# Kernel tuning notes

Measured on AMD Instinct MI355X. Metric: run time of the kernel, lower is better.

The kernel has to match this reference:

```python
import jax, jax.numpy as jnp
import numpy as np

NUM_NODES = 50000
NUM_EDGES = 800000
DIM = 64
NUM_REL2 = 400
NUM_LAYERS = 3
NUM_TAILS = 512


def setup_inputs() -> dict:
    key = jax.random.key(0)
    ks = jax.random.split(key, 16)
    s = lambda shape, k, scale: jax.random.normal(k, shape, jnp.float32) * scale
    return {
        'head_embeds': s((DIM,), ks[0], 1.0),
        'rel_table': s((NUM_REL2, DIM), ks[1], 0.1),
        'rel_W': s((NUM_LAYERS, NUM_REL2, DIM), ks[2], 0.1),
        'agg_W': s((NUM_LAYERS, 8 * DIM, DIM), ks[3], (8 * DIM) ** -0.5),
        'agg_b': jnp.zeros((NUM_LAYERS, DIM), jnp.float32),
        'lin_W': s((2 * DIM, DIM), ks[4], (2 * DIM) ** -0.5),
        'lin_b': jnp.zeros((DIM,), jnp.float32),
        'mlp_W1': s((DIM, 2 * DIM), ks[5], DIM ** -0.5),
        'mlp_b1': jnp.zeros((2 * DIM,), jnp.float32),
        'mlp_W2': s((2 * DIM, 1), ks[6], (2 * DIM) ** -0.5),
        'mlp_b2': jnp.zeros((1,), jnp.float32),
        'edge_src': jax.random.randint(ks[7], (NUM_EDGES,), 0, NUM_NODES, jnp.int32),
        'edge_dst': jax.random.randint(ks[8], (NUM_EDGES,), 0, NUM_NODES, jnp.int32),
        'edge_type': jax.random.randint(ks[9], (NUM_EDGES,), 0, NUM_REL2, jnp.int32),
        'head_index': 0,
        'r_index': 7,
        't_index': jax.random.randint(ks[10], (NUM_TAILS,), 0, NUM_NODES, jnp.int32),
    }


def _score_fn(hidden, query, lin_W, lin_b, mlp_W1, mlp_b1, mlp_W2, mlp_b2):
    # hidden: [N, d], query: [d]
    q = jnp.broadcast_to(query, hidden.shape)
    heuristic = jnp.concatenate([hidden, q], axis=-1) @ lin_W + lin_b  # [N, d]
    x = hidden * heuristic
    h1 = jax.nn.relu(x @ mlp_W1 + mlp_b1)
    return (h1 @ mlp_W2 + mlp_b2)[..., 0]  # [N]


def reference(head_embeds, rel_table, rel_W, agg_W, agg_b, lin_W, lin_b,
              mlp_W1, mlp_b1, mlp_W2, mlp_b2,
              edge_src, edge_dst, edge_type, head_index, r_index, t_index):
    N, d = NUM_NODES, DIM
    score_fn = lambda h, q: _score_fn(h, q, lin_W, lin_b, mlp_W1, mlp_b1, mlp_W2, mlp_b2)

    query = rel_table[r_index]  # [d]

    # init_input_embeds: boundary zeros except head node; init score
    hidden = jnp.zeros((N, d), jnp.float32).at[head_index].set(head_embeds)
    zero_s = score_fn(jnp.zeros((1, d), jnp.float32), query)[0]
    score = jnp.full((N,), zero_s, jnp.float32)
    score = score.at[head_index].set(score_fn(head_embeds[None, :], query)[0])
    score = jnp.clip(score, -15.0, 15.0)

    deg = jax.ops.segment_sum(jnp.ones_like(edge_dst, jnp.float32), edge_dst, N)  # [N]
    deg_safe = jnp.maximum(deg, 1.0)
    has_in = deg > 0
    pna_degree_mean = jnp.log(deg + 1.0).mean()
    scale = (jnp.log(deg + 1.0) / pna_degree_mean)[:, None]  # [N,1]

    for l in range(NUM_LAYERS):
        gate = jax.nn.sigmoid(score)[:, None]  # [N,1]
        layer_input = gate * hidden  # [N,d]
        # relational messages: gather + per-relation transform
        msg = layer_input[edge_src] * rel_W[l][edge_type]  # [E,d]
        # PNA aggregators per destination node
        ssum = jax.ops.segment_sum(msg, edge_dst, N)
        mean = ssum / deg_safe[:, None]
        sq = jax.ops.segment_sum(msg * msg, edge_dst, N) / deg_safe[:, None]
        std = jnp.sqrt(jnp.maximum(sq - mean * mean, 0.0) + 1e-6)
        mx = jax.ops.segment_max(msg, edge_dst, N)
        mn = jax.ops.segment_min(msg, edge_dst, N)
        mx = jnp.where(has_in[:, None], mx, 0.0)
        mn = jnp.where(has_in[:, None], mn, 0.0)
        feat = jnp.concatenate([mean, mx, mn, std], axis=-1)  # [N,4d]
        feat = jnp.concatenate([feat, feat * scale], axis=-1)  # [N,8d]
        update = feat @ agg_W[l] + agg_b[l]  # [N,d]
        # residual update only for nodes with incoming edges
        hidden = hidden + jnp.where(has_in[:, None], update, 0.0)
        new_score = score_fn(hidden, query)
        score = jnp.where(has_in, new_score, score)

    return score[t_index]  # [NUM_TAILS]
```

## Files before the change

kernel.cpp:

```cpp
#include <hip/hip_runtime.h>
#include <math.h>

#define NN 50000
#define NREL 400
#define NLAYERS 3

static __device__ __forceinline__ float clip15(float x) { return fminf(fmaxf(x, -15.f), 15.f); }

__global__ void count_k(const int* __restrict__ dst, int* __restrict__ deg, int E) {
  int e = blockIdx.x * blockDim.x + threadIdx.x;
  if (e < E) atomicAdd(&deg[dst[e]], 1);
}

__global__ void scan_k(const int* __restrict__ deg, int* __restrict__ start, int* __restrict__ cursor,
                       int* __restrict__ counter, float* __restrict__ logsum, int N) {
  int n = blockIdx.x * blockDim.x + threadIdx.x;
  int lane = threadIdx.x & 63;
  int d = (n < N) ? deg[n] : 0;
  int pre = d;
  #pragma unroll
  for (int off = 1; off < 64; off <<= 1) { int t = __shfl_up(pre, off); if (lane >= off) pre += t; }
  int base = 0;
  if (lane == 63) base = atomicAdd(counter, pre);
  base = __shfl(base, 63);
  if (n < N) { int pos = base + pre - d; start[n] = pos; cursor[n] = pos; }
  float v = (n < N) ? logf((float)d + 1.0f) : 0.f;
  #pragma unroll
  for (int off = 32; off; off >>= 1) v += __shfl_xor(v, off);
  if (lane == 0) atomicAdd(logsum, v);
}

__global__ void scale_k(const int* __restrict__ deg, const float* __restrict__ logsum,
                        float* __restrict__ scale, int N) {
  int n = blockIdx.x * blockDim.x + threadIdx.x;
  if (n < N) scale[n] = logf((float)deg[n] + 1.0f) * (float)N / logsum[0];
}

__global__ void scatter_k(const int* __restrict__ src, const int* __restrict__ dst,
                          const int* __restrict__ typ, int* __restrict__ cursor,
                          int2* __restrict__ csr, int E) {
  int e = blockIdx.x * blockDim.x + threadIdx.x;
  if (e < E) {
    int dd = dst[e];
    int pos = atomicAdd(&cursor[dd], 1);
    csr[pos] = make_int2(src[e], typ[e]);
  }
}

__global__ void prep_k(const float* __restrict__ head_embeds, const float* __restrict__ rel_table,
                       const float* __restrict__ lin_W, const float* __restrict__ lin_b,
                       const float* __restrict__ mlp_W1, const float* __restrict__ mlp_b1,
                       const float* __restrict__ mlp_W2, const float* __restrict__ mlp_b2,
                       const int* __restrict__ head_index, const int* __restrict__ r_index,
                       float* __restrict__ hidden, float* __restrict__ scalars) {
  int j = threadIdx.x;
  int r = r_index[0], hd = head_index[0];
  float qj = rel_table[r * 64 + j];
  float cq = lin_b[j];
  for (int k = 0; k < 64; ++k) cq += __shfl(qj, k) * lin_W[(64 + k) * 64 + j];
  scalars[j] = cq;
  float t = fmaxf(mlp_b1[j], 0.f) * mlp_W2[j] + fmaxf(mlp_b1[64 + j], 0.f) * mlp_W2[64 + j];
  #pragma unroll
  for (int off = 32; off; off >>= 1) t += __shfl_xor(t, off);
  float zs = clip15(t + mlp_b2[0]);
  float hj = head_embeds[j];
  hidden[(size_t)hd * 64 + j] = hj;
  float heur = cq;
  for (int k = 0; k < 64; ++k) heur += __shfl(hj, k) * lin_W[k * 64 + j];
  float xj = hj * heur;
  float h1a = mlp_b1[j], h1b = mlp_b1[64 + j];
  for (int k = 0; k < 64; ++k) {
    float xk = __shfl(xj, k);
    h1a += xk * mlp_W1[k * 128 + j];
    h1b += xk * mlp_W1[k * 128 + 64 + j];
  }
  h1a = fmaxf(h1a, 0.f); h1b = fmaxf(h1b, 0.f);
  float p = h1a * mlp_W2[j] + h1b * mlp_W2[64 + j];
  #pragma unroll
  for (int off = 32; off; off >>= 1) p += __shfl_xor(p, off);
  float hs = clip15(p + mlp_b2[0]);
  if (j == 0) { scalars[64] = zs; scalars[65] = hs; }
}

__global__ void fill_k(float* __restrict__ score, const float* __restrict__ scalars,
                       const int* __restrict__ head_index, int N) {
  int n = blockIdx.x * blockDim.x + threadIdx.x;
  if (n < N) score[n] = (n == head_index[0]) ? scalars[65] : scalars[64];
}

__global__ void gate_k(const float* __restrict__ hidden, const float* __restrict__ score,
                       float* __restrict__ LI, int N) {
  int i = blockIdx.x * blockDim.x + threadIdx.x;
  if (i < N * 16) {
    int node = i >> 4;
    float s = score[node];
    float g = 1.f / (1.f + expf(-s));
    float4 h = ((const float4*)hidden)[i];
    float4 r = make_float4(h.x * g, h.y * g, h.z * g, h.w * g);
    ((float4*)LI)[i] = r;
  }
}

__global__ __launch_bounds__(256) void agg_k(const float* __restrict__ LI, const int2* __restrict__ csr,
                                             const int* __restrict__ start, const int* __restrict__ deg,
                                             const float* __restrict__ relW, float* __restrict__ f1, int N) {
  int wid = threadIdx.x >> 6;
  int lane = threadIdx.x & 63;
  int node = blockIdx.x * 4 + wid;
  if (node >= N) return;
  int base = start[node], d = deg[node];
  float sum = 0.f, sq = 0.f, mx = -3.402823e38f, mn = 3.402823e38f;
  int e = 0;
  for (; e + 8 <= d; e += 8) {
    int2 p[8];
    #pragma unroll
    for (int i = 0; i < 8; ++i) p[i] = csr[base + e + i];
    float m[8];
    #pragma unroll
    for (int i = 0; i < 8; ++i) {
      float a = LI[p[i].x * 64 + lane];
      float w = relW[p[i].y * 64 + lane];
      m[i] = a * w;
    }
    #pragma unroll
    for (int i = 0; i < 8; ++i) {
      sum += m[i]; sq += m[i] * m[i];
      mx = fmaxf(mx, m[i]); mn = fminf(mn, m[i]);
    }
  }
  for (; e + 4 <= d; e += 4) {
    int2 p0 = csr[base + e], p1 = csr[base + e + 1];
    int2 p2 = csr[base + e + 2], p3 = csr[base + e + 3];
    float a0 = LI[p0.x * 64 + lane], w0 = relW[p0.y * 64 + lane];
    float a1 = LI[p1.x * 64 + lane], w1 = relW[p1.y * 64 + lane];
    float a2 = LI[p2.x * 64 + lane], w2 = relW[p2.y * 64 + lane];
    float a3 = LI[p3.x * 64 + lane], w3 = relW[p3.y * 64 + lane];
    float m0 = a0 * w0, m1 = a1 * w1, m2 = a2 * w2, m3 = a3 * w3;
    sum += (m0 + m1) + (m2 + m3);
    sq += (m0 * m0 + m1 * m1) + (m2 * m2 + m3 * m3);
    mx = fmaxf(fmaxf(mx, fmaxf(m0, m1)), fmaxf(m2, m3));
    mn = fminf(fminf(mn, fminf(m0, m1)), fminf(m2, m3));
  }
  for (; e < d; ++e) {
    int2 p = csr[base + e];
    float m = LI[p.x * 64 + lane] * relW[p.y * 64 + lane];
    sum += m; sq += m * m; mx = fmaxf(mx, m); mn = fminf(mn, m);
  }
  float* out = f1 + (size_t)node * 256;
  if (d > 0) {
    float inv = 1.0f / (float)d;
    float mean = sum * inv, sqm = sq * inv;
    float sd = sqrtf(fmaxf(sqm - mean * mean, 0.f) + 1e-6f);
    out[lane] = mean; out[64 + lane] = mx; out[128 + lane] = mn; out[192 + lane] = sd;
  } else {
    out[lane] = 0.f; out[64 + lane] = 0.f; out[128 + lane] = 0.f; out[192 + lane] = 0.f;
  }
}

__global__ __launch_bounds__(256) void gemm_k(const float* __restrict__ f1, const float* __restrict__ aggW,
                                              const float* __restrict__ aggb, const float* __restrict__ scale,
                                              const int* __restrict__ deg, float* __restrict__ hidden, int N) {
  __shared__ float At[32][68];
  __shared__ float Was[32][64];
  __shared__ float Wbs[32][64];
  int tid = threadIdx.x;
  int tx = tid & 15;
  int tn = tid >> 4;
  int n0 = blockIdx.x * 64;
  float acc_a[4][4] = {{0.f}}, acc_b[4][4] = {{0.f}};
  int anode = tid >> 2;
  int ak = (tid & 3) * 8;
  bool avalid = (n0 + anode) < N;
  const float* Arow = f1 + (size_t)(n0 + anode) * 256 + ak;
  const float4* WaG = (const float4*)(aggW);
  const float4* WbG = (const float4*)(aggW + (size_t)256 * 64);
  for (int kc = 0; kc < 8; ++kc) {
    float4 v0 = make_float4(0.f, 0.f, 0.f, 0.f), v1 = v0;
    if (avalid) {
      const float4* ap = (const float4*)(Arow + kc * 32);
      v0 = ap[0]; v1 = ap[1];
    }
    At[ak + 0][anode] = v0.x; At[ak + 1][anode] = v0.y;
    At[ak + 2][anode] = v0.z; At[ak + 3][anode] = v0.w;
    At[ak + 4][anode] = v1.x; At[ak + 5][anode] = v1.y;
    At[ak + 6][anode] = v1.z; At[ak + 7][anode] = v1.w;
    ((float4*)Was)[tid] = WaG[kc * 512 + tid];
    ((float4*)Was)[tid + 256] = WaG[kc * 512 + 256 + tid];
    ((float4*)Wbs)[tid] = WbG[kc * 512 + tid];
    ((float4*)Wbs)[tid + 256] = WbG[kc * 512 + 256 + tid];
    __syncthreads();
    #pragma unroll 8
    for (int kk = 0; kk < 32; ++kk) {
      float4 a  = *(const float4*)&At[kk][tn * 4];
      float4 wa = *(const float4*)&Was[kk][tx * 4];
      float4 wb = *(const float4*)&Wbs[kk][tx * 4];
      acc_a[0][0] += a.x * wa.x; acc_a[0][1] += a.x * wa.y; acc_a[0][2] += a.x * wa.z; acc_a[0][3] += a.x * wa.w;
      acc_a[1][0] += a.y * wa.x; acc_a[1][1] += a.y * wa.y; acc_a[1][2] += a.y * wa.z; acc_a[1][3] += a.y * wa.w;
      acc_a[2][0] += a.z * wa.x; acc_a[2][1] += a.z * wa.y; acc_a[2][2] += a.z * wa.z; acc_a[2][3] += a.z * wa.w;
      acc_a[3][0] += a.w * wa.x; acc_a[3][1] += a.w * wa.y; acc_a[3][2] += a.w * wa.z; acc_a[3][3] += a.w * wa.w;
      acc_b[0][0] += a.x * wb.x; acc_b[0][1] += a.x * wb.y; acc_b[0][2] += a.x * wb.z; acc_b[0][3] += a.x * wb.w;
      acc_b[1][0] += a.y * wb.x; acc_b[1][1] += a.y * wb.y; acc_b[1][2] += a.y * wb.z; acc_b[1][3] += a.y * wb.w;
      acc_b[2][0] += a.z * wb.x; acc_b[2][1] += a.z * wb.y; acc_b[2][2] += a.z * wb.z; acc_b[2][3] += a.z * wb.w;
      acc_b[3][0] += a.w * wb.x; acc_b[3][1] += a.w * wb.y; acc_b[3][2] += a.w * wb.z; acc_b[3][3] += a.w * wb.w;
    }
    __syncthreads();
  }
  float4 bj = *(const float4*)(aggb + tx * 4);
  #pragma unroll
  for (int i = 0; i < 4; ++i) {
    int node = n0 + tn * 4 + i;
    if (node < N && deg[node] > 0) {
      float sc = scale[node];
      float4* hp = (float4*)(hidden + (size_t)node * 64 + tx * 4);
      float4 h = *hp;
      h.x += acc_a[i][0] + sc * acc_b[i][0] + bj.x;
      h.y += acc_a[i][1] + sc * acc_b[i][1] + bj.y;
      h.z += acc_a[i][2] + sc * acc_b[i][2] + bj.z;
      h.w += acc_a[i][3] + sc * acc_b[i][3] + bj.w;
      *hp = h;
    }
  }
}

#define SC_LDS 12992
__global__ __launch_bounds__(256) void score2_k(const float* __restrict__ hidden, float* __restrict__ score,
                                                const int* __restrict__ deg, const float* __restrict__ lin_W,
                                                const float* __restrict__ mlp_W1, const float* __restrict__ mlp_b1,
                                                const float* __restrict__ mlp_W2, const float* __restrict__ mlp_b2,
                                                const float* __restrict__ scalars, int N) {
  __shared__ float smem[SC_LDS];
  float* X   = smem;
  float* H   = smem + 4160;
  float* WA  = smem + 8320;
  float* W1s = smem + 4160;
  float* sW2 = smem + 12416;
  float* sb1 = smem + 12544;
  float* scq = smem + 12672;
  float* pred= smem + 12736;

  int t = threadIdx.x;
  int lane = t & 63;
  int g = t >> 6;
  int n0 = blockIdx.x * 64;

  for (int i = t; i < 1024; i += 256) ((float4*)WA)[i] = ((const float4*)lin_W)[i];
  if (t < 128) { sW2[t] = mlp_W2[t]; sb1[t] = mlp_b1[t]; }
  if (t < 64) scq[t] = scalars[t];
  for (int i = t; i < 1024; i += 256) {
    int node = i >> 4;
    int k4 = (i & 15) << 2;
    float4 v = make_float4(0.f, 0.f, 0.f, 0.f);
    if (n0 + node < N) v = ((const float4*)(hidden + (size_t)(n0 + node) * 64))[i & 15];
    float* hp = &H[node * 65 + k4];
    hp[0] = v.x; hp[1] = v.y; hp[2] = v.z; hp[3] = v.w;
  }
  __syncthreads();

  float acc[16];
  #pragma unroll
  for (int i = 0; i < 16; ++i) acc[i] = scq[g * 16 + i];
  #pragma unroll 8
  for (int kk = 0; kk < 64; ++kk) {
    float h = H[lane * 65 + kk];
    const float4* wr = (const float4*)&WA[kk * 64 + g * 16];
    float4 w0 = wr[0], w1 = wr[1], w2 = wr[2], w3 = wr[3];
    acc[0]  += h * w0.x; acc[1]  += h * w0.y; acc[2]  += h * w0.z; acc[3]  += h * w0.w;
    acc[4]  += h * w1.x; acc[5]  += h * w1.y; acc[6]  += h * w1.z; acc[7]  += h * w1.w;
    acc[8]  += h * w2.x; acc[9]  += h * w2.y; acc[10] += h * w2.z; acc[11] += h * w2.w;
    acc[12] += h * w3.x; acc[13] += h * w3.y; acc[14] += h * w3.z; acc[15] += h * w3.w;
  }
  #pragma unroll
  for (int i = 0; i < 16; ++i) {
    int j = g * 16 + i;
    X[lane * 65 + j] = H[lane * 65 + j] * acc[i];
  }
  __syncthreads();

  for (int i = t; i < 2048; i += 256) ((float4*)W1s)[i] = ((const float4*)mlp_W1)[i];
  __syncthreads();

  float acc2[32];
  #pragma unroll
  for (int i = 0; i < 32; ++i) acc2[i] = sb1[g * 32 + i];
  #pragma unroll 4
  for (int kk = 0; kk < 64; ++kk) {
    float xv = X[lane * 65 + kk];
    const float4* wr = (const float4*)&W1s[kk * 128 + g * 32];
    #pragma unroll
    for (int s = 0; s < 8; ++s) {
      float4 w = wr[s];
      acc2[s * 4 + 0] += xv * w.x; acc2[s * 4 + 1] += xv * w.y;
      acc2[s * 4 + 2] += xv * w.z; acc2[s * 4 + 3] += xv * w.w;
    }
  }
  float p = 0.f;
  #pragma unroll
  for (int i = 0; i < 32; ++i) p += fmaxf(acc2[i], 0.f) * sW2[g * 32 + i];
  pred[g * 64 + lane] = p;
  __syncthreads();
  if (t < 64) {
    int node = n0 + t;
    if (node < N && deg[node] > 0)
      score[node] = pred[t] + pred[64 + t] + pred[128 + t] + pred[192 + t] + mlp_b2[0];
  }
}

__global__ void out_k(const float* __restrict__ score, const int* __restrict__ t_index,
                      float* __restrict__ out, int T) {
  int i = blockIdx.x * blockDim.x + threadIdx.x;
  if (i < T) out[i] = score[t_index[i]];
}

extern "C" void kernel_launch(void* const* d_in, const int* in_sizes, int n_in,
                              void* d_out, int out_size, void* d_ws, size_t ws_size,
                              hipStream_t stream) {
  const float* head_embeds = (const float*)d_in[0];
  const float* rel_table   = (const float*)d_in[1];
  const float* rel_W       = (const float*)d_in[2];
  const float* agg_W       = (const float*)d_in[3];
  const float* agg_b       = (const float*)d_in[4];
  const float* lin_W       = (const float*)d_in[5];
  const float* lin_b       = (const float*)d_in[6];
  const float* mlp_W1      = (const float*)d_in[7];
  const float* mlp_b1      = (const float*)d_in[8];
  const float* mlp_W2      = (const float*)d_in[9];
  const float* mlp_b2      = (const float*)d_in[10];
  const int* edge_src      = (const int*)d_in[11];
  const int* edge_dst      = (const int*)d_in[12];
  const int* edge_type     = (const int*)d_in[13];
  const int* head_index    = (const int*)d_in[14];
  const int* r_index       = (const int*)d_in[15];
  const int* t_index       = (const int*)d_in[16];
  int E = in_sizes[11];
  int T = in_sizes[16];
  int N = NN;

  char* w = (char*)d_ws;
  size_t off = 0;
  auto alloc = [&](size_t bytes) {
    void* p = w + off;
    off = (off + bytes + 255) & ~(size_t)255;
    return p;
  };
  int* deg      = (int*)alloc((size_t)N * 4);
  int* start    = (int*)alloc((size_t)N * 4);
  int* cursor   = (int*)alloc((size_t)N * 4);
  float* scale  = (float*)alloc((size_t)N * 4);
  int* counter  = (int*)alloc(4);
  float* logsum = (float*)alloc(4);
  float* scalars= (float*)alloc(66 * 4);
  int2* csr     = (int2*)alloc((size_t)E * 8);
  float* hidden = (float*)alloc((size_t)N * 64 * 4);
  float* score  = (float*)alloc((size_t)N * 4);
  float* LI     = (float*)alloc((size_t)N * 64 * 4);
  float* f1     = (float*)alloc((size_t)N * 256 * 4);
  if (off > ws_size) return;

  hipMemsetAsync(deg, 0, (size_t)N * 4, stream);
  hipMemsetAsync(counter, 0, 4, stream);
  hipMemsetAsync(logsum, 0, 4, stream);
  hipMemsetAsync(hidden, 0, (size_t)N * 64 * 4, stream);

  count_k<<<(E + 255) / 256, 256, 0, stream>>>(edge_dst, deg, E);
  scan_k<<<(N + 255) / 256, 256, 0, stream>>>(deg, start, cursor, counter, logsum, N);
  scale_k<<<(N + 255) / 256, 256, 0, stream>>>(deg, logsum, scale, N);
  scatter_k<<<(E + 255) / 256, 256, 0, stream>>>(edge_src, edge_dst, edge_type, cursor, csr, E);
  prep_k<<<1, 64, 0, stream>>>(head_embeds, rel_table, lin_W, lin_b, mlp_W1, mlp_b1, mlp_W2, mlp_b2,
                               head_index, r_index, hidden, scalars);
  fill_k<<<(N + 255) / 256, 256, 0, stream>>>(score, scalars, head_index, N);

  for (int l = 0; l < NLAYERS; ++l) {
    gate_k<<<(N * 16 + 255) / 256, 256, 0, stream>>>(hidden, score, LI, N);
    agg_k<<<(N + 3) / 4, 256, 0, stream>>>(LI, csr, start, deg, rel_W + (size_t)l * NREL * 64, f1, N);
    gemm_k<<<(N + 63) / 64, 256, 0, stream>>>(f1, agg_W + (size_t)l * 512 * 64, agg_b + (size_t)l * 64,
                                              scale, deg, hidden, N);
    score2_k<<<(N + 63) / 64, 256, 0, stream>>>(hidden, score, deg, lin_W, mlp_W1, mlp_b1, mlp_W2, mlp_b2,
                                                scalars, N);
  }
  out_k<<<(T + 255) / 256, 256, 0, stream>>>(score, t_index, (float*)d_out, T);
}
```

Baseline: 586.2 us.

## Use split-bf16 MFMA for aggregation GEMM instead of FP32 FMA

Replaces the FP32 scalar-FMA tiled GEMM with bf16 MFMA 16x16x32 instructions. Both activations and weights are split into high and low bf16 parts, and three products are accumulated to approximate FP32 accuracy. A one-time kernel converts and transposes agg_W into hi/lo bf16 planes. The aim is to move the dense 256x128 per-node GEMM onto matrix cores. The cost is extra conversion ALU work, more LDS traffic and per-element scalar writes in the epilogue.

```diff
diff --git a/kernel.cpp b/kernel.cpp
--- a/kernel.cpp
+++ b/kernel.cpp
@@ -6,6 +6,18 @@
 #define NLAYERS 3
 
 static __device__ __forceinline__ float clip15(float x) { return fminf(fmaxf(x, -15.f), 15.f); }
+
+static __device__ __forceinline__ unsigned short f2bf(float f) {
+  unsigned u = __float_as_uint(f);
+  unsigned r = (u + 0x7FFFu + ((u >> 16) & 1u)) >> 16;
+  return (unsigned short)r;
+}
+static __device__ __forceinline__ float bf2f(unsigned short s) {
+  return __uint_as_float(((unsigned)s) << 16);
+}
+
+typedef __attribute__((ext_vector_type(8))) short bf16x8;
+typedef __attribute__((ext_vector_type(4))) float f32x4;
 
 __global__ void count_k(const int* __restrict__ dst, int* __restrict__ deg, int E) {
   int e = blockIdx.x * blockDim.x + threadIdx.x;
@@ -45,6 +57,26 @@
     int pos = atomicAdd(&cursor[dd], 1);
     csr[pos] = make_int2(src[e], typ[e]);
   }
+}
+
+__global__ void wconv_k(const float* __restrict__ aggW, unsigned short* __restrict__ WT) {
+  int idx = blockIdx.x * blockDim.x + threadIdx.x;
+  if (idx >= 3 * 64 * 256) return;
+  int k = idx & 255;
+  int out = (idx >> 8) & 63;
+  int l = idx >> 14;
+  const float* Wl = aggW + (size_t)l * 512 * 64;
+  float wa = Wl[(size_t)k * 64 + out];
+  float wb = Wl[(size_t)(256 + k) * 64 + out];
+  unsigned short wah = f2bf(wa);
+  unsigned short wal = f2bf(wa - bf2f(wah));
+  unsigned short wbh = f2bf(wb);
+  unsigned short wbl = f2bf(wb - bf2f(wbh));
+  unsigned short* WTl = WT + (size_t)l * 4 * 64 * 256;
+  WTl[((size_t)0 * 64 + out) * 256 + k] = wah;
+  WTl[((size_t)1 * 64 + out) * 256 + k] = wal;
+  WTl[((size_t)2 * 64 + out) * 256 + k] = wbh;
+  WTl[((size_t)3 * 64 + out) * 256 + k] = wbl;
 }
 
 __global__ void prep_k(const float* __restrict__ head_embeds, const float* __restrict__ rel_table,
@@ -157,67 +189,93 @@
   }
 }
 
-__global__ __launch_bounds__(256) void gemm_k(const float* __restrict__ f1, const float* __restrict__ aggW,
+#define KP 40
+__global__ __launch_bounds__(256) void gemm_k(const float* __restrict__ f1,
+                                              const unsigned short* __restrict__ WT,
                                               const float* __restrict__ aggb, const float* __restrict__ scale,
                                               const int* __restrict__ deg, float* __restrict__ hidden, int N) {
-  __shared__ float At[32][68];
-  __shared__ float Was[32][64];
-  __shared__ float Wbs[32][64];
+  __shared__ __align__(16) unsigned short sA[2][64 * KP];
+  __shared__ __align__(16) unsigned short sW[4][64 * KP];
   int tid = threadIdx.x;
-  int tx = tid & 15;
-  int tn = tid >> 4;
+  int wv = tid >> 6;
+  int l = tid & 63;
+  int lrow = l & 15;
+  int lhi = l >> 4;
   int n0 = blockIdx.x * 64;
-  float acc_a[4][4] = {{0.f}}, acc_b[4][4] = {{0.f}};
+
+  f32x4 acc[8];
+  #pragma unroll
+  for (int i = 0; i < 8; ++i) acc[i] = (f32x4){0.f, 0.f, 0.f, 0.f};
+
   int anode = tid >> 2;
-  int ak = (tid & 3) * 8;
+  int akq = (tid & 3) * 8;
   bool avalid = (n0 + anode) < N;
-  const float* Arow = f1 + (size_t)(n0 + anode) * 256 + ak;
-  const float4* WaG = (const float4*)(aggW);
-  const float4* WbG = (const float4*)(aggW + (size_t)256 * 64);
+  const float* Arow = f1 + (size_t)(n0 + anode) * 256 + akq;
+
   for (int kc = 0; kc < 8; ++kc) {
-    float4 v0 = make_float4(0.f, 0.f, 0.f, 0.f), v1 = v0;
+    float fv[8];
     if (avalid) {
-      const float4* ap = (const float4*)(Arow + kc * 32);
-      v0 = ap[0]; v1 = ap[1];
-    }
-    At[ak + 0][anode] = v0.x; At[ak + 1][anode] = v0.y;
-    At[ak + 2][anode] = v0.z; At[ak + 3][anode] = v0.w;
-    At[ak + 4][anode] = v1.x; At[ak + 5][anode] = v1.y;
-    At[ak + 6][anode] = v1.z; At[ak + 7][anode] = v1.w;
-    ((float4*)Was)[tid] = WaG[kc * 512 + tid];
-    ((float4*)Was)[tid + 256] = WaG[kc * 512 + 256 + tid];
-    ((float4*)Wbs)[tid] = WbG[kc * 512 + tid];
-    ((float4*)Wbs)[tid + 256] = WbG[kc * 512 + 256 + tid];
+      float4 v0 = *(const float4*)(Arow + kc * 32);
+      float4 v1 = *(const float4*)(Arow + kc * 32 + 4);
+      fv[0] = v0.x; fv[1] = v0.y; fv[2] = v0.z; fv[3] = v0.w;
+      fv[4] = v1.x; fv[5] = v1.y; fv[6] = v1.z; fv[7] = v1.w;
+    } else {
+      #pragma unroll
+      for (int j = 0; j < 8; ++j) fv[j] = 0.f;
+    }
+    unsigned int ph[4], pl[4];
+    #pragma unroll
+    for (int j = 0; j < 4; ++j) {
+      unsigned short h0 = f2bf(fv[2 * j]),     l0 = f2bf(fv[2 * j] - bf2f(h0));
+      unsigned short h1 = f2bf(fv[2 * j + 1]), l1 = f2bf(fv[2 * j + 1] - bf2f(h1));
+      ph[j] = (unsigned)h0 | ((unsigned)h1 << 16);
+      pl[j] = (unsigned)l0 | ((unsigned)l1 << 16);
+    }
+    *(uint4*)&sA[0][anode * KP + akq] = make_uint4(ph[0], ph[1], ph[2], ph[3]);
+    *(uint4*)&sA[1][anode * KP + akq] = make_uint4(pl[0], pl[1], pl[2], pl[3]);
+    {
+      int wrow = tid >> 2;
+      int wkq = (tid & 3) * 8;
+      #pragma unroll
+      for (int p = 0; p < 4; ++p) {
+        const unsigned short* src = WT + ((size_t)p * 64 + wrow) * 256 + kc * 32 + wkq;
+        *(uint4*)&sW[p][wrow * KP + wkq] = *(const uint4*)src;
+      }
+    }
     __syncthreads();
-    #pragma unroll 8
-    for (int kk = 0; kk < 32; ++kk) {
-      float4 a  = *(const float4*)&At[kk][tn * 4];
-      float4 wa = *(const float4*)&Was[kk][tx * 4];
-      float4 wb = *(const float4*)&Wbs[kk][tx * 4];
-      acc_a[0][0] += a.x * wa.x; acc_a[0][1] += a.x * wa.y; acc_a[0][2] += a.x * wa.z; acc_a[0][3] += a.x * wa.w;
-      acc_a[1][0] += a.y * wa.x; acc_a[1][1] += a.y * wa.y; acc_a[1][2] += a.y * wa.z; acc_a[1][3] += a.y * wa.w;
-      acc_a[2][0] += a.z * wa.x; acc_a[2][1] += a.z * wa.y; acc_a[2][2] += a.z * wa.z; acc_a[2][3] += a.z * wa.w;
-      acc_a[3][0] += a.w * wa.x; acc_a[3][1] += a.w * wa.y; acc_a[3][2] += a.w * wa.z; acc_a[3][3] += a.w * wa.w;
-      acc_b[0][0] += a.x * wb.x; acc_b[0][1] += a.x * wb.y; acc_b[0][2] += a.x * wb.z; acc_b[0][3] += a.x * wb.w;
-      acc_b[1][0] += a.y * wb.x; acc_b[1][1] += a.y * wb.y; acc_b[1][2] += a.y * wb.z; acc_b[1][3] += a.y * wb.w;
-      acc_b[2][0] += a.z * wb.x; acc_b[2][1] += a.z * wb.y; acc_b[2][2] += a.z * wb.z; acc_b[2][3] += a.z * wb.w;
-      acc_b[3][0] += a.w * wb.x; acc_b[3][1] += a.w * wb.y; acc_b[3][2] += a.w * wb.z; acc_b[3][3] += a.w * wb.w;
+    {
+      int arow = (wv * 16 + lrow) * KP + lhi * 8;
+      bf16x8 ah = *(const bf16x8*)&sA[0][arow];
+      bf16x8 al = *(const bf16x8*)&sA[1][arow];
+      #pragma unroll
+      for (int t = 0; t < 4; ++t) {
+        int wr = (t * 16 + lrow) * KP + lhi * 8;
+        bf16x8 wah = *(const bf16x8*)&sW[0][wr];
+        bf16x8 wal = *(const bf16x8*)&sW[1][wr];
+        acc[t] = __builtin_amdgcn_mfma_f32_16x16x32_bf16(ah, wah, acc[t], 0, 0, 0);
+        acc[t] = __builtin_amdgcn_mfma_f32_16x16x32_bf16(ah, wal, acc[t], 0, 0, 0);
+        acc[t] = __builtin_amdgcn_mfma_f32_16x16x32_bf16(al, wah, acc[t], 0, 0, 0);
+        bf16x8 wbh = *(const bf16x8*)&sW[2][wr];
+        bf16x8 wbl = *(const bf16x8*)&sW[3][wr];
+        acc[4 + t] = __builtin_amdgcn_mfma_f32_16x16x32_bf16(ah, wbh, acc[4 + t], 0, 0, 0);
+        acc[4 + t] = __builtin_amdgcn_mfma_f32_16x16x32_bf16(ah, wbl, acc[4 + t], 0, 0, 0);
+        acc[4 + t] = __builtin_amdgcn_mfma_f32_16x16x32_bf16(al, wbh, acc[4 + t], 0, 0, 0);
+      }
     }
     __syncthreads();
   }
-  float4 bj = *(const float4*)(aggb + tx * 4);
-  #pragma unroll
-  for (int i = 0; i < 4; ++i) {
-    int node = n0 + tn * 4 + i;
+
+  #pragma unroll
+  for (int r = 0; r < 4; ++r) {
+    int node = n0 + wv * 16 + lhi * 4 + r;
     if (node < N && deg[node] > 0) {
       float sc = scale[node];
-      float4* hp = (float4*)(hidden + (size_t)node * 64 + tx * 4);
-      float4 h = *hp;
-      h.x += acc_a[i][0] + sc * acc_b[i][0] + bj.x;
-      h.y += acc_a[i][1] + sc * acc_b[i][1] + bj.y;
-      h.z += acc_a[i][2] + sc * acc_b[i][2] + bj.z;
-      h.w += acc_a[i][3] + sc * acc_b[i][3] + bj.w;
-      *hp = h;
+      #pragma unroll
+      for (int t = 0; t < 4; ++t) {
+        int out = t * 16 + lrow;
+        float* hp = &hidden[(size_t)node * 64 + out];
+        *hp += acc[t][r] + sc * acc[4 + t][r] + aggb[out];
+      }
     }
   }
 }
@@ -354,6 +412,7 @@
   float* score  = (float*)alloc((size_t)N * 4);
   float* LI     = (float*)alloc((size_t)N * 64 * 4);
   float* f1     = (float*)alloc((size_t)N * 256 * 4);
+  unsigned short* WT = (unsigned short*)alloc((size_t)3 * 4 * 64 * 256 * 2);
   if (off > ws_size) return;
 
   hipMemsetAsync(deg, 0, (size_t)N * 4, stream);
@@ -365,6 +424,7 @@
   scan_k<<<(N + 255) / 256, 256, 0, stream>>>(deg, start, cursor, counter, logsum, N);
   scale_k<<<(N + 255) / 256, 256, 0, stream>>>(deg, logsum, scale, N);
   scatter_k<<<(E + 255) / 256, 256, 0, stream>>>(edge_src, edge_dst, edge_type, cursor, csr, E);
+  wconv_k<<<(3 * 64 * 256 + 255) / 256, 256, 0, stream>>>(agg_W, WT);
   prep_k<<<1, 64, 0, stream>>>(head_embeds, rel_table, lin_W, lin_b, mlp_W1, mlp_b1, mlp_W2, mlp_b2,
                                head_index, r_index, hidden, scalars);
   fill_k<<<(N + 255) / 256, 256, 0, stream>>>(score, scalars, head_index, N);
@@ -372,8 +432,8 @@
   for (int l = 0; l < NLAYERS; ++l) {
     gate_k<<<(N * 16 + 255) / 256, 256, 0, stream>>>(hidden, score, LI, N);
     agg_k<<<(N + 3) / 4, 256, 0, stream>>>(LI, csr, start, deg, rel_W + (size_t)l * NREL * 64, f1, N);
-    gemm_k<<<(N + 63) / 64, 256, 0, stream>>>(f1, agg_W + (size_t)l * 512 * 64, agg_b + (size_t)l * 64,
-                                              scale, deg, hidden, N);
+    gemm_k<<<(N + 63) / 64, 256, 0, stream>>>(f1, WT + (size_t)l * 4 * 64 * 256,
+                                              agg_b + (size_t)l * 64, scale, deg, hidden, N);
     score2_k<<<(N + 63) / 64, 256, 0, stream>>>(hidden, score, deg, lin_W, mlp_W1, mlp_b1, mlp_W2, mlp_b2,
                                                 scalars, N);
   }
```

Result: faster. 504.2 us (-14.0%).
